# Performance work log

Measured on AMD Instinct MI355X. Metric: run time of the kernel, lower is better.

Reference implementation:

```python
import jax, jax.numpy as jnp
import numpy as np

N_NODES = 100000


def gcn_conv(x, W, b, src, dst, n_nodes):
    """PyG GCNConv: add self-loops, symmetric normalization, linear, scatter-add, bias."""
    xw = x @ W  # [N, out]
    loop = jnp.arange(n_nodes, dtype=src.dtype)
    src2 = jnp.concatenate([src, loop])  # sources (x_j gathered from here)
    dst2 = jnp.concatenate([dst, loop])  # targets (aggregation index)
    # degree (incl. self-loops) computed at target nodes, unit edge weights
    deg = jax.ops.segment_sum(jnp.ones_like(dst2, dtype=xw.dtype), dst2, num_segments=n_nodes)
    dinv = jnp.where(deg > 0, jax.lax.rsqrt(deg), 0.0)
    norm = dinv[src2] * dinv[dst2]  # [E+N]
    msg = xw[src2] * norm[:, None]  # [E+N, out]  (memory-bound gather)
    out = jax.ops.segment_sum(msg, dst2, num_segments=n_nodes)  # scatter-add
    return out + b


def setup_inputs() -> dict:
    key = jax.random.key(0)
    k1, k2, k3, k4 = jax.random.split(key, 4)
    F_IN, H, C = 128, 128, 64
    E = 1600000
    x = jax.random.normal(k1, (N_NODES, F_IN), dtype=jnp.float32)
    edge_index = jax.random.randint(k2, (2, E), 0, N_NODES, dtype=jnp.int64)
    # Glorot init like PyG GCNConv
    s1 = float(np.sqrt(6.0 / (F_IN + H)))
    s2 = float(np.sqrt(6.0 / (H + C)))
    W1 = jax.random.uniform(k3, (F_IN, H), jnp.float32, -s1, s1)
    W2 = jax.random.uniform(k4, (H, C), jnp.float32, -s2, s2)
    b1 = jnp.zeros((H,), jnp.float32)
    b2 = jnp.zeros((C,), jnp.float32)
    return {"x": x, "edge_index": edge_index, "W1": W1, "b1": b1, "W2": W2, "b2": b2}


def reference(x, edge_index, W1, b1, W2, b2):
    src, dst = edge_index[0], edge_index[1]
    h = gcn_conv(x, W1, b1, src, dst, N_NODES)
    h = jax.nn.relu(h)  # dropout p=0.0 -> identity
    h = gcn_conv(h, W2, b2, src, dst, N_NODES)
    return jax.nn.log_softmax(h, axis=1)
```

## Files before the change

### kernel.cpp

```cpp
#include <hip/hip_runtime.h>
#include <cmath>


#define THREADS 256
#define BSHIFT 8
#define MAXB 512
#define PADSLACK 1792

__device__ __forceinline__ unsigned short f2bf(float f) {
    union { float f; unsigned u; } v; v.f = f;
    unsigned r = v.u + 0x7FFFu + ((v.u >> 16) & 1u);
    return (unsigned short)(r >> 16);
}
__device__ __forceinline__ float bf_lo(unsigned u) {
    union { unsigned u; float f; } v; v.u = u << 16; return v.f;
}
__device__ __forceinline__ float bf_hi(unsigned u) {
    union { unsigned u; float f; } v; v.u = u & 0xFFFF0000u; return v.f;
}

__global__ __launch_bounds__(256) void k_bcount(const int* __restrict__ dst, int E, int B,
                                                int* __restrict__ bcnt) {
    __shared__ int lc[MAXB];
    for (int i = threadIdx.x; i < MAXB; i += 256) lc[i] = 0;
    __syncthreads();
    for (int e = blockIdx.x * blockDim.x + threadIdx.x; e < E; e += gridDim.x * blockDim.x)
        atomicAdd(&lc[dst[e] >> BSHIFT], 1);
    __syncthreads();
    for (int b = threadIdx.x; b < B; b += 256)
        if (lc[b]) atomicAdd(&bcnt[b], lc[b]);
}

__global__ void k_bscan(const int* __restrict__ bcnt, int B, int* __restrict__ boff) {
    __shared__ int sh[MAXB];
    const int t = threadIdx.x;
    int v = (t < B) ? bcnt[t] : 0;
    sh[t] = v; __syncthreads();
    for (int o = 1; o < MAXB; o <<= 1) {
        int add = (t >= o) ? sh[t - o] : 0;
        __syncthreads();
        sh[t] += add;
        __syncthreads();
    }
    if (t < B) boff[t] = sh[t] - v;
    if (t == B - 1) boff[B] = sh[t];
}

__global__ __launch_bounds__(256) void k_bscatter(const int* __restrict__ src,
                                                  const int* __restrict__ dst, int E, int B,
                                                  const int* __restrict__ boff,
                                                  int* __restrict__ bfill,
                                                  unsigned* __restrict__ pairs) {
    __shared__ int lc[MAXB];
    __shared__ int lbase[MAXB];
    const int tid = threadIdx.x;
    const int e0 = blockIdx.x * 8192;
    for (int i = tid; i < MAXB; i += 256) lc[i] = 0;
    __syncthreads();
#pragma unroll
    for (int k = 0; k < 32; k++) {
        int e = e0 + k * 256 + tid;
        if (e < E) atomicAdd(&lc[dst[e] >> BSHIFT], 1);
    }
    __syncthreads();
    for (int b = tid; b < B; b += 256)
        lbase[b] = lc[b] ? atomicAdd(&bfill[b], lc[b]) : 0;
    __syncthreads();
    for (int i = tid; i < MAXB; i += 256) lc[i] = 0;
    __syncthreads();
#pragma unroll
    for (int k = 0; k < 32; k++) {
        int e = e0 + k * 256 + tid;
        if (e < E) {
            int s = src[e], d = dst[e];
            int b = d >> BSHIFT;
            int r = atomicAdd(&lc[b], 1);
            pairs[(size_t)boff[b] + lbase[b] + r] =
                ((unsigned)(d & 255) << 24) | (unsigned)s;
        }
    }
}

__global__ __launch_bounds__(256) void k_bbuild(const unsigned* __restrict__ pairs,
                                                const int* __restrict__ boff, int N,
                                                int* __restrict__ deg,
                                                float* __restrict__ dinv,
                                                int* __restrict__ rowptr,
                                                int* __restrict__ csr_src) {
    __shared__ int ldeg[256], lex[256], lrank[256];
    const int b = blockIdx.x, tid = threadIdx.x;
    const int node0 = b << BSHIFT;
    const int base = boff[b];
    const int pbase = base + b * PADSLACK;
    const int cnt_e = boff[b + 1] - base;
    ldeg[tid] = 0;
    __syncthreads();
    for (int e = tid; e < cnt_e; e += 256)
        atomicAdd(&ldeg[pairs[base + e] >> 24], 1);
    __syncthreads();
    int v = ldeg[tid];
    int pd = (v + 7) & ~7;
    lex[tid] = pd; __syncthreads();
    for (int o = 1; o < 256; o <<= 1) {
        int add = (tid >= o) ? lex[tid - o] : 0;
        __syncthreads();
        lex[tid] += add;
        __syncthreads();
    }
    int pexcl = lex[tid] - pd;
    if (node0 + tid < N) {
        deg[node0 + tid] = v;
        dinv[node0 + tid] = rsqrtf((float)(v + 1));
        rowptr[node0 + tid] = pbase + pexcl;
    }
    __syncthreads();
    lex[tid] = pexcl;
    lrank[tid] = 0;
    __syncthreads();
    for (int e = tid; e < cnt_e; e += 256) {
        unsigned p = pairs[base + e];
        int loc = p >> 24;
        int r = atomicAdd(&lrank[loc], 1);
        csr_src[pbase + lex[loc] + r] = (int)(p & 0xFFFFFFu);
    }
    for (int p = v; p < pd; p++)
        csr_src[pbase + pexcl + p] = N;
}

__global__ void k_castW(const float* __restrict__ W1, const float* __restrict__ W2,
                        unsigned short* __restrict__ Wt1, unsigned short* __restrict__ Wt2) {
    int idx = blockIdx.x * blockDim.x + threadIdx.x;
    if (idx < 16384) {
        int n = idx >> 7, k = idx & 127;
        Wt1[idx] = f2bf(W1[k * 128 + n]);
    } else if (idx < 16384 + 8192) {
        int t = idx - 16384;
        int n = t >> 7, k = t & 127;
        Wt2[t] = f2bf(W2[k * 64 + n]);
    }
}

typedef __attribute__((ext_vector_type(8))) short bf16x8;
typedef __attribute__((ext_vector_type(4))) float f32x4;

template <int NC, bool A_BF16>
__global__ __launch_bounds__(256) void k_gemm_mfma(const void* __restrict__ Av,
                                                   const unsigned short* __restrict__ Wt,
                                                   const float* __restrict__ dinv,
                                                   unsigned short* __restrict__ Out,
                                                   unsigned short* __restrict__ zrow,
                                                   int M) {
    constexpr int KP = 136;
    __shared__ __align__(16) short As[64 * KP];
    __shared__ __align__(16) short Bs[NC * KP];
    const int tid = threadIdx.x;
    const int row0 = blockIdx.x * 64;

    if (blockIdx.x == 0 && tid < NC) zrow[tid] = 0;

    if (A_BF16) {
        const unsigned short* A = (const unsigned short*)Av;
#pragma unroll
        for (int q = 0; q < 4; q++) {
            int f = tid + 256 * q;
            int r = f >> 4, c = (f & 15) * 8;
            uint4 v = make_uint4(0, 0, 0, 0);
            if (row0 + r < M) v = *(const uint4*)&A[(size_t)(row0 + r) * 128 + c];
            *(uint4*)&As[r * KP + c] = v;
        }
    } else {
        const float* A = (const float*)Av;
#pragma unroll
        for (int q = 0; q < 8; q++) {
            int f = tid + 256 * q;
            int r = f >> 5, c = (f & 31) * 4;
            float4 v = make_float4(0.f, 0.f, 0.f, 0.f);
            if (row0 + r < M) v = *(const float4*)&A[(size_t)(row0 + r) * 128 + c];
            ushort4 o;
            o.x = f2bf(v.x); o.y = f2bf(v.y); o.z = f2bf(v.z); o.w = f2bf(v.w);
            *(ushort4*)&As[r * KP + c] = o;
        }
    }
    for (int f = tid; f < NC * 16; f += 256) {
        int n = f >> 4, c = (f & 15) * 8;
        *(uint4*)&Bs[n * KP + c] = *(const uint4*)&Wt[n * 128 + c];
    }
    __syncthreads();

    const int wave = tid >> 6, lane = tid & 63;
    const int m = lane & 15, quad = lane >> 4;
    constexpr int CT = NC / 16;
    f32x4 acc[CT] = {};
    const short* arow = &As[(16 * wave + m) * KP + quad * 8];
    const short* brow = &Bs[m * KP + quad * 8];
#pragma unroll
    for (int k0 = 0; k0 < 128; k0 += 32) {
        bf16x8 a = *(const bf16x8*)&arow[k0];
#pragma unroll
        for (int c = 0; c < CT; c++) {
            bf16x8 b = *(const bf16x8*)&brow[(size_t)c * 16 * KP + k0];
            acc[c] = __builtin_amdgcn_mfma_f32_16x16x32_bf16(a, b, acc[c], 0, 0, 0);
        }
    }

    __syncthreads();
    short* Cs = As;
    const int rbase = 16 * wave + quad * 4;
    float dv[4];
#pragma unroll
    for (int r = 0; r < 4; r++) {
        int gr = row0 + rbase + r;
        dv[r] = dinv[gr < M ? gr : 0];
    }
#pragma unroll
    for (int c = 0; c < CT; c++)
#pragma unroll
        for (int r = 0; r < 4; r++)
            Cs[(rbase + r) * NC + 16 * c + m] = (short)f2bf(acc[c][r] * dv[r]);
    __syncthreads();
    for (int f = tid; f < 64 * NC / 8; f += 256) {
        int r = f / (NC / 8), c = (f % (NC / 8)) * 8;
        if (row0 + r < M)
            *(uint4*)&Out[(size_t)(row0 + r) * NC + c] = *(const uint4*)&Cs[r * NC + c];
    }
}

__global__ __launch_bounds__(256) void k_agg128b(const int* __restrict__ csr_src,
                                                 const int* __restrict__ rowptr,
                                                 const int* __restrict__ cnt,
                                                 const float* __restrict__ dinv,
                                                 const unsigned* __restrict__ xw,
                                                 const float* __restrict__ bias,
                                                 unsigned* __restrict__ h1, int N) {
    const int lane = threadIdx.x & 63;
    const int wid = (blockIdx.x * blockDim.x + threadIdx.x) >> 6;
    const int h = lane >> 5, sl = lane & 31;
    const int i = wid * 2 + h;
    if (i >= N) return;
    const float di = dinv[i];
    uint2 u = *(const uint2*)&xw[(size_t)i * 64 + 2 * sl];
    float a0 = bf_lo(u.x), a1 = bf_hi(u.x);
    float a2 = bf_lo(u.y), a3 = bf_hi(u.y);
    const int start = rowptr[i];
    const int pc = (cnt[i] + 7) & ~7;
    int s[8];
#pragma unroll
    for (int k = 0; k < 8; k++) s[k] = csr_src[start + k];
    for (int j = 0; j < pc; j += 8) {
        uint2 uu[8];
#pragma unroll
        for (int k = 0; k < 8; k++) uu[k] = *(const uint2*)&xw[(size_t)s[k] * 64 + 2 * sl];
#pragma unroll
        for (int k = 0; k < 8; k++) s[k] = csr_src[start + j + 8 + k];
#pragma unroll
        for (int k = 0; k < 8; k++) {
            a0 += bf_lo(uu[k].x); a1 += bf_hi(uu[k].x);
            a2 += bf_lo(uu[k].y); a3 += bf_hi(uu[k].y);
        }
    }
    float4 b = *(const float4*)&bias[4 * sl];
    float r0 = fmaxf(di * a0 + b.x, 0.f);
    float r1 = fmaxf(di * a1 + b.y, 0.f);
    float r2 = fmaxf(di * a2 + b.z, 0.f);
    float r3 = fmaxf(di * a3 + b.w, 0.f);
    uint2 o;
    o.x = (unsigned)f2bf(r0) | ((unsigned)f2bf(r1) << 16);
    o.y = (unsigned)f2bf(r2) | ((unsigned)f2bf(r3) << 16);
    *(uint2*)&h1[(size_t)i * 64 + 2 * sl] = o;
}

__global__ __launch_bounds__(256) void k_agg64b(const int* __restrict__ csr_src,
                                                const int* __restrict__ rowptr,
                                                const int* __restrict__ cnt,
                                                const float* __restrict__ dinv,
                                                const unsigned* __restrict__ xw,
                                                const float* __restrict__ bias,
                                                float* __restrict__ out, int N) {
    const int lane = threadIdx.x & 63;
    const int wid = (blockIdx.x * blockDim.x + threadIdx.x) >> 6;
    const int h = lane >> 5;
    const int q = (lane >> 4) & 1;
    const int sl = lane & 15;
    const int i = wid * 2 + h;
    if (i >= N) return;
    const float di = dinv[i];
    float a0 = 0.f, a1 = 0.f, a2 = 0.f, a3 = 0.f;
    if (q == 0) {
        uint2 u = *(const uint2*)&xw[(size_t)i * 32 + 2 * sl];
        a0 = bf_lo(u.x); a1 = bf_hi(u.x); a2 = bf_lo(u.y); a3 = bf_hi(u.y);
    }
    const int start = rowptr[i];
    const int pc = (cnt[i] + 7) & ~7;
    int s[4];
#pragma unroll
    for (int k = 0; k < 4; k++) s[k] = csr_src[start + q + 2 * k];
    for (int e = 0; e < pc; e += 8) {
        uint2 uu[4];
#pragma unroll
        for (int k = 0; k < 4; k++) uu[k] = *(const uint2*)&xw[(size_t)s[k] * 32 + 2 * sl];
#pragma unroll
        for (int k = 0; k < 4; k++) s[k] = csr_src[start + e + 8 + q + 2 * k];
#pragma unroll
        for (int k = 0; k < 4; k++) {
            a0 += bf_lo(uu[k].x); a1 += bf_hi(uu[k].x);
            a2 += bf_lo(uu[k].y); a3 += bf_hi(uu[k].y);
        }
    }
    a0 += __shfl_xor(a0, 16); a1 += __shfl_xor(a1, 16);
    a2 += __shfl_xor(a2, 16); a3 += __shfl_xor(a3, 16);
    float4 b = *(const float4*)&bias[4 * sl];
    float v0 = di * a0 + b.x, v1 = di * a1 + b.y;
    float v2 = di * a2 + b.z, v3 = di * a3 + b.w;
    float m = fmaxf(fmaxf(v0, v1), fmaxf(v2, v3));
#pragma unroll
    for (int o = 8; o > 0; o >>= 1) m = fmaxf(m, __shfl_xor(m, o));
    float s2 = expf(v0 - m) + expf(v1 - m) + expf(v2 - m) + expf(v3 - m);
#pragma unroll
    for (int o = 8; o > 0; o >>= 1) s2 += __shfl_xor(s2, o);
    float ls = m + logf(s2);
    if (q == 0)
        *(float4*)&out[(size_t)i * 64 + 4 * sl] =
            make_float4(v0 - ls, v1 - ls, v2 - ls, v3 - ls);
}

extern "C" void kernel_launch(void* const* d_in, const int* in_sizes, int n_in,
                              void* d_out, int out_size, void* d_ws, size_t ws_size,
                              hipStream_t stream) {
    const float* x  = (const float*)d_in[0];
    const int*   ei = (const int*)d_in[1];
    const float* W1 = (const float*)d_in[2];
    const float* b1 = (const float*)d_in[3];
    const float* W2 = (const float*)d_in[4];
    const float* b2 = (const float*)d_in[5];

    const int N = in_sizes[0] / 128;
    const int E = in_sizes[1] / 2;
    const int* src = ei;
    const int* dst = ei + E;
    const int B = (N + 255) >> BSHIFT;

    char* ws = (char*)d_ws;
    size_t off = 0;
    auto alloc = [&](size_t bytes) {
        void* p = ws + off;
        off += (bytes + 255) & ~(size_t)255;
        return p;
    };
    int*            bcnt    = (int*)alloc(MAXB * 4 * 2);
    int*            bfill   = bcnt + MAXB;
    int*            boff    = (int*)alloc((MAXB + 1) * 4);
    int*            deg     = (int*)alloc((size_t)N * 4);
    float*          dinv    = (float*)alloc((size_t)N * 4);
    int*            rowptr  = (int*)alloc((size_t)N * 4);
    int*            csr_src = (int*)alloc(((size_t)E + (size_t)B * PADSLACK + 64) * 4);
    unsigned*       pairs   = (unsigned*)alloc((size_t)E * 4);
    unsigned short* Wt1     = (unsigned short*)alloc(128 * 128 * 2);
    unsigned short* Wt2     = (unsigned short*)alloc(64 * 128 * 2);
    unsigned short* xw1     = (unsigned short*)alloc((size_t)(N + 1) * 128 * 2);
    unsigned short* h1      = (unsigned short*)alloc((size_t)N * 128 * 2);
    unsigned short* hw2     = xw1;
    float*          out     = (float*)d_out;

    hipMemsetAsync(bcnt, 0, MAXB * 4 * 2, stream);

    k_bcount<<<512, THREADS, 0, stream>>>(dst, E, B, bcnt);
    k_bscan<<<1, MAXB, 0, stream>>>(bcnt, B, boff);
    k_bscatter<<<(E + 8191) / 8192, THREADS, 0, stream>>>(src, dst, E, B, boff, bfill, pairs);
    k_bbuild<<<B, THREADS, 0, stream>>>(pairs, boff, N, deg, dinv, rowptr, csr_src);

    k_castW<<<96, THREADS, 0, stream>>>(W1, W2, Wt1, Wt2);

    const int aggBlocks = (N + 7) / 8;

    k_gemm_mfma<128, false><<<(N + 63) / 64, THREADS, 0, stream>>>(
        x, Wt1, dinv, xw1, xw1 + (size_t)N * 128, N);
    k_agg128b<<<aggBlocks, THREADS, 0, stream>>>(
        csr_src, rowptr, deg, dinv, (const unsigned*)xw1, b1, (unsigned*)h1, N);

    k_gemm_mfma<64, true><<<(N + 63) / 64, THREADS, 0, stream>>>(
        h1, Wt2, dinv, hw2, hw2 + (size_t)N * 64, N);
    k_agg64b<<<aggBlocks, THREADS, 0, stream>>>(
        csr_src, rowptr, deg, dinv, (const unsigned*)hw2, b2, out, N);
}
```

Baseline: 287.3 us.

## Store CSR byte offsets, widen aggregation loads, feed GEMM A directly from registers

The CSR build now stores each source index pre-shifted as a byte offset into the bf16 feature table, so the gather kernels skip the index multiply. Both aggregation kernels switch to 16-byte loads with 16 or 8 lanes per node, so each wave handles 4 or 8 nodes; in the second layer this also removes the split-edge cross-lane shuffle. The MFMA GEMM loads its A fragments straight from global memory into registers instead of staging them through LDS, and reuses the B buffer for the output tile. The aim is fewer, wider memory transactions and less LDS traffic, at the cost of more registers and less coalesced A loads.

New measurement: 275.0 us. -4.3%, faster.

```diff
diff --git a/kernel.cpp b/kernel.cpp
--- a/kernel.cpp
+++ b/kernel.cpp
@@ -86,7 +86,7 @@
                                                 int* __restrict__ deg,
                                                 float* __restrict__ dinv,
                                                 int* __restrict__ rowptr,
-                                                int* __restrict__ csr_src) {
+                                                unsigned* __restrict__ csr_off) {
     __shared__ int ldeg[256], lex[256], lrank[256];
     const int b = blockIdx.x, tid = threadIdx.x;
     const int node0 = b << BSHIFT;
@@ -121,10 +121,10 @@
         unsigned p = pairs[base + e];
         int loc = p >> 24;
         int r = atomicAdd(&lrank[loc], 1);
-        csr_src[pbase + lex[loc] + r] = (int)(p & 0xFFFFFFu);
+        csr_off[pbase + lex[loc] + r] = (p & 0xFFFFFFu) << 8;
     }
     for (int p = v; p < pd; p++)
-        csr_src[pbase + pexcl + p] = N;
+        csr_off[pbase + pexcl + p] = ((unsigned)N) << 8;
 }
 
 __global__ void k_castW(const float* __restrict__ W1, const float* __restrict__ W2,
@@ -151,60 +151,58 @@
                                                    unsigned short* __restrict__ zrow,
                                                    int M) {
     constexpr int KP = 136;
-    __shared__ __align__(16) short As[64 * KP];
     __shared__ __align__(16) short Bs[NC * KP];
     const int tid = threadIdx.x;
     const int row0 = blockIdx.x * 64;
 
     if (blockIdx.x == 0 && tid < NC) zrow[tid] = 0;
 
-    if (A_BF16) {
-        const unsigned short* A = (const unsigned short*)Av;
-#pragma unroll
-        for (int q = 0; q < 4; q++) {
-            int f = tid + 256 * q;
-            int r = f >> 4, c = (f & 15) * 8;
-            uint4 v = make_uint4(0, 0, 0, 0);
-            if (row0 + r < M) v = *(const uint4*)&A[(size_t)(row0 + r) * 128 + c];
-            *(uint4*)&As[r * KP + c] = v;
-        }
-    } else {
-        const float* A = (const float*)Av;
-#pragma unroll
-        for (int q = 0; q < 8; q++) {
-            int f = tid + 256 * q;
-            int r = f >> 5, c = (f & 31) * 4;
-            float4 v = make_float4(0.f, 0.f, 0.f, 0.f);
-            if (row0 + r < M) v = *(const float4*)&A[(size_t)(row0 + r) * 128 + c];
-            ushort4 o;
-            o.x = f2bf(v.x); o.y = f2bf(v.y); o.z = f2bf(v.z); o.w = f2bf(v.w);
-            *(ushort4*)&As[r * KP + c] = o;
-        }
-    }
     for (int f = tid; f < NC * 16; f += 256) {
         int n = f >> 4, c = (f & 15) * 8;
         *(uint4*)&Bs[n * KP + c] = *(const uint4*)&Wt[n * 128 + c];
     }
-    __syncthreads();
 
     const int wave = tid >> 6, lane = tid & 63;
     const int m = lane & 15, quad = lane >> 4;
+    const int row = row0 + 16 * wave + m;
+    const int rowc = row < M ? row : (M - 1);
+
+    bf16x8 afr[4];
+    if (A_BF16) {
+        const unsigned short* A = (const unsigned short*)Av;
+#pragma unroll
+        for (int k = 0; k < 4; k++)
+            afr[k] = *(const bf16x8*)&A[(size_t)rowc * 128 + quad * 8 + 32 * k];
+    } else {
+        const float* A = (const float*)Av;
+#pragma unroll
+        for (int k = 0; k < 4; k++) {
+            float4 lo = *(const float4*)&A[(size_t)rowc * 128 + quad * 8 + 32 * k];
+            float4 hi = *(const float4*)&A[(size_t)rowc * 128 + quad * 8 + 32 * k + 4];
+            bf16x8 a;
+            a[0] = (short)f2bf(lo.x); a[1] = (short)f2bf(lo.y);
+            a[2] = (short)f2bf(lo.z); a[3] = (short)f2bf(lo.w);
+            a[4] = (short)f2bf(hi.x); a[5] = (short)f2bf(hi.y);
+            a[6] = (short)f2bf(hi.z); a[7] = (short)f2bf(hi.w);
+            afr[k] = a;
+        }
+    }
+    __syncthreads();
+
     constexpr int CT = NC / 16;
     f32x4 acc[CT] = {};
-    const short* arow = &As[(16 * wave + m) * KP + quad * 8];
     const short* brow = &Bs[m * KP + quad * 8];
 #pragma unroll
-    for (int k0 = 0; k0 < 128; k0 += 32) {
-        bf16x8 a = *(const bf16x8*)&arow[k0];
+    for (int k = 0; k < 4; k++) {
 #pragma unroll
         for (int c = 0; c < CT; c++) {
-            bf16x8 b = *(const bf16x8*)&brow[(size_t)c * 16 * KP + k0];
-            acc[c] = __builtin_amdgcn_mfma_f32_16x16x32_bf16(a, b, acc[c], 0, 0, 0);
-        }
-    }
-
-    __syncthreads();
-    short* Cs = As;
+            bf16x8 b = *(const bf16x8*)&brow[(size_t)c * 16 * KP + 32 * k];
+            acc[c] = __builtin_amdgcn_mfma_f32_16x16x32_bf16(afr[k], b, acc[c], 0, 0, 0);
+        }
+    }
+
+    __syncthreads();
+    short* Cs = Bs;
     const int rbase = 16 * wave + quad * 4;
     float dv[4];
 #pragma unroll
@@ -225,102 +223,113 @@
     }
 }
 
-__global__ __launch_bounds__(256) void k_agg128b(const int* __restrict__ csr_src,
+__global__ __launch_bounds__(256) void k_agg128b(const unsigned* __restrict__ csr_off,
                                                  const int* __restrict__ rowptr,
                                                  const int* __restrict__ cnt,
                                                  const float* __restrict__ dinv,
-                                                 const unsigned* __restrict__ xw,
+                                                 const unsigned char* __restrict__ xwb,
                                                  const float* __restrict__ bias,
                                                  unsigned* __restrict__ h1, int N) {
     const int lane = threadIdx.x & 63;
     const int wid = (blockIdx.x * blockDim.x + threadIdx.x) >> 6;
-    const int h = lane >> 5, sl = lane & 31;
-    const int i = wid * 2 + h;
+    const int g = lane >> 4, sl = lane & 15;
+    const int i = wid * 4 + g;
     if (i >= N) return;
     const float di = dinv[i];
-    uint2 u = *(const uint2*)&xw[(size_t)i * 64 + 2 * sl];
-    float a0 = bf_lo(u.x), a1 = bf_hi(u.x);
-    float a2 = bf_lo(u.y), a3 = bf_hi(u.y);
+    const int slb = sl * 16;
+    uint4 u = *(const uint4*)(xwb + ((size_t)i << 8) + slb);
+    float a0 = bf_lo(u.x), a1 = bf_hi(u.x), a2 = bf_lo(u.y), a3 = bf_hi(u.y);
+    float a4 = bf_lo(u.z), a5 = bf_hi(u.z), a6 = bf_lo(u.w), a7 = bf_hi(u.w);
     const int start = rowptr[i];
     const int pc = (cnt[i] + 7) & ~7;
-    int s[8];
-#pragma unroll
-    for (int k = 0; k < 8; k++) s[k] = csr_src[start + k];
+    unsigned s[8];
+#pragma unroll
+    for (int k = 0; k < 8; k++) s[k] = csr_off[start + k];
     for (int j = 0; j < pc; j += 8) {
-        uint2 uu[8];
-#pragma unroll
-        for (int k = 0; k < 8; k++) uu[k] = *(const uint2*)&xw[(size_t)s[k] * 64 + 2 * sl];
-#pragma unroll
-        for (int k = 0; k < 8; k++) s[k] = csr_src[start + j + 8 + k];
+        uint4 uu[8];
+#pragma unroll
+        for (int k = 0; k < 8; k++) uu[k] = *(const uint4*)(xwb + s[k] + slb);
+#pragma unroll
+        for (int k = 0; k < 8; k++) s[k] = csr_off[start + j + 8 + k];
 #pragma unroll
         for (int k = 0; k < 8; k++) {
             a0 += bf_lo(uu[k].x); a1 += bf_hi(uu[k].x);
             a2 += bf_lo(uu[k].y); a3 += bf_hi(uu[k].y);
-        }
-    }
-    float4 b = *(const float4*)&bias[4 * sl];
-    float r0 = fmaxf(di * a0 + b.x, 0.f);
-    float r1 = fmaxf(di * a1 + b.y, 0.f);
-    float r2 = fmaxf(di * a2 + b.z, 0.f);
-    float r3 = fmaxf(di * a3 + b.w, 0.f);
-    uint2 o;
+            a4 += bf_lo(uu[k].z); a5 += bf_hi(uu[k].z);
+            a6 += bf_lo(uu[k].w); a7 += bf_hi(uu[k].w);
+        }
+    }
+    float4 b0 = *(const float4*)&bias[8 * sl];
+    float4 b1 = *(const float4*)&bias[8 * sl + 4];
+    float r0 = fmaxf(di * a0 + b0.x, 0.f);
+    float r1 = fmaxf(di * a1 + b0.y, 0.f);
+    float r2 = fmaxf(di * a2 + b0.z, 0.f);
+    float r3 = fmaxf(di * a3 + b0.w, 0.f);
+    float r4 = fmaxf(di * a4 + b1.x, 0.f);
+    float r5 = fmaxf(di * a5 + b1.y, 0.f);
+    float r6 = fmaxf(di * a6 + b1.z, 0.f);
+    float r7 = fmaxf(di * a7 + b1.w, 0.f);
+    uint4 o;
     o.x = (unsigned)f2bf(r0) | ((unsigned)f2bf(r1) << 16);
     o.y = (unsigned)f2bf(r2) | ((unsigned)f2bf(r3) << 16);
-    *(uint2*)&h1[(size_t)i * 64 + 2 * sl] = o;
-}
-
-__global__ __launch_bounds__(256) void k_agg64b(const int* __restrict__ csr_src,
+    o.z = (unsigned)f2bf(r4) | ((unsigned)f2bf(r5) << 16);
+    o.w = (unsigned)f2bf(r6) | ((unsigned)f2bf(r7) << 16);
+    *(uint4*)&h1[(size_t)i * 64 + 4 * sl] = o;
+}
+
+__global__ __launch_bounds__(256) void k_agg64b(const unsigned* __restrict__ csr_off,
                                                 const int* __restrict__ rowptr,
                                                 const int* __restrict__ cnt,
                                                 const float* __restrict__ dinv,
-                                                const unsigned* __restrict__ xw,
+                                                const unsigned char* __restrict__ xwb,
                                                 const float* __restrict__ bias,
                                                 float* __restrict__ out, int N) {
     const int lane = threadIdx.x & 63;
     const int wid = (blockIdx.x * blockDim.x + threadIdx.x) >> 6;
-    const int h = lane >> 5;
-    const int q = (lane >> 4) & 1;
-    const int sl = lane & 15;
-    const int i = wid * 2 + h;
+    const int g = lane >> 3, sl = lane & 7;
+    const int i = wid * 8 + g;
     if (i >= N) return;
     const float di = dinv[i];
-    float a0 = 0.f, a1 = 0.f, a2 = 0.f, a3 = 0.f;
-    if (q == 0) {
-        uint2 u = *(const uint2*)&xw[(size_t)i * 32 + 2 * sl];
-        a0 = bf_lo(u.x); a1 = bf_hi(u.x); a2 = bf_lo(u.y); a3 = bf_hi(u.y);
-    }
+    const int slb = sl * 16;
+    uint4 u = *(const uint4*)(xwb + ((size_t)i << 7) + slb);
+    float a0 = bf_lo(u.x), a1 = bf_hi(u.x), a2 = bf_lo(u.y), a3 = bf_hi(u.y);
+    float a4 = bf_lo(u.z), a5 = bf_hi(u.z), a6 = bf_lo(u.w), a7 = bf_hi(u.w);
     const int start = rowptr[i];
     const int pc = (cnt[i] + 7) & ~7;
-    int s[4];
-#pragma unroll
-    for (int k = 0; k < 4; k++) s[k] = csr_src[start + q + 2 * k];
-    for (int e = 0; e < pc; e += 8) {
-        uint2 uu[4];
-#pragma unroll
-        for (int k = 0; k < 4; k++) uu[k] = *(const uint2*)&xw[(size_t)s[k] * 32 + 2 * sl];
-#pragma unroll
-        for (int k = 0; k < 4; k++) s[k] = csr_src[start + e + 8 + q + 2 * k];
-#pragma unroll
-        for (int k = 0; k < 4; k++) {
+    unsigned s[8];
+#pragma unroll
+    for (int k = 0; k < 8; k++) s[k] = csr_off[start + k];
+    for (int j = 0; j < pc; j += 8) {
+        uint4 uu[8];
+#pragma unroll
+        for (int k = 0; k < 8; k++) uu[k] = *(const uint4*)(xwb + (s[k] >> 1) + slb);
+#pragma unroll
+        for (int k = 0; k < 8; k++) s[k] = csr_off[start + j + 8 + k];
+#pragma unroll
+        for (int k = 0; k < 8; k++) {
             a0 += bf_lo(uu[k].x); a1 += bf_hi(uu[k].x);
             a2 += bf_lo(uu[k].y); a3 += bf_hi(uu[k].y);
-        }
-    }
-    a0 += __shfl_xor(a0, 16); a1 += __shfl_xor(a1, 16);
-    a2 += __shfl_xor(a2, 16); a3 += __shfl_xor(a3, 16);
-    float4 b = *(const float4*)&bias[4 * sl];
-    float v0 = di * a0 + b.x, v1 = di * a1 + b.y;
-    float v2 = di * a2 + b.z, v3 = di * a3 + b.w;
-    float m = fmaxf(fmaxf(v0, v1), fmaxf(v2, v3));
-#pragma unroll
-    for (int o = 8; o > 0; o >>= 1) m = fmaxf(m, __shfl_xor(m, o));
-    float s2 = expf(v0 - m) + expf(v1 - m) + expf(v2 - m) + expf(v3 - m);
-#pragma unroll
-    for (int o = 8; o > 0; o >>= 1) s2 += __shfl_xor(s2, o);
+            a4 += bf_lo(uu[k].z); a5 += bf_hi(uu[k].z);
+            a6 += bf_lo(uu[k].w); a7 += bf_hi(uu[k].w);
+        }
+    }
+    float4 b0 = *(const float4*)&bias[8 * sl];
+    float4 b1 = *(const float4*)&bias[8 * sl + 4];
+    float v0 = di * a0 + b0.x, v1 = di * a1 + b0.y;
+    float v2 = di * a2 + b0.z, v3 = di * a3 + b0.w;
+    float v4 = di * a4 + b1.x, v5 = di * a5 + b1.y;
+    float v6 = di * a6 + b1.z, v7 = di * a7 + b1.w;
+    float m = fmaxf(fmaxf(fmaxf(v0, v1), fmaxf(v2, v3)),
+                    fmaxf(fmaxf(v4, v5), fmaxf(v6, v7)));
+#pragma unroll
+    for (int o = 4; o > 0; o >>= 1) m = fmaxf(m, __shfl_xor(m, o));
+    float s2 = expf(v0 - m) + expf(v1 - m) + expf(v2 - m) + expf(v3 - m) +
+               expf(v4 - m) + expf(v5 - m) + expf(v6 - m) + expf(v7 - m);
+#pragma unroll
+    for (int o = 4; o > 0; o >>= 1) s2 += __shfl_xor(s2, o);
     float ls = m + logf(s2);
-    if (q == 0)
-        *(float4*)&out[(size_t)i * 64 + 4 * sl] =
-            make_float4(v0 - ls, v1 - ls, v2 - ls, v3 - ls);
+    *(float4*)&out[(size_t)i * 64 + 8 * sl] = make_float4(v0 - ls, v1 - ls, v2 - ls, v3 - ls);
+    *(float4*)&out[(size_t)i * 64 + 8 * sl + 4] = make_float4(v4 - ls, v5 - ls, v6 - ls, v7 - ls);
 }
 
 extern "C" void kernel_launch(void* const* d_in, const int* in_sizes, int n_in,
@@ -352,7 +361,7 @@
     int*            deg     = (int*)alloc((size_t)N * 4);
     float*          dinv    = (float*)alloc((size_t)N * 4);
     int*            rowptr  = (int*)alloc((size_t)N * 4);
-    int*            csr_src = (int*)alloc(((size_t)E + (size_t)B * PADSLACK + 64) * 4);
+    unsigned*       csr_off = (unsigned*)alloc(((size_t)E + (size_t)B * PADSLACK + 64) * 4);
     unsigned*       pairs   = (unsigned*)alloc((size_t)E * 4);
     unsigned short* Wt1     = (unsigned short*)alloc(128 * 128 * 2);
     unsigned short* Wt2     = (unsigned short*)alloc(64 * 128 * 2);
@@ -366,19 +375,20 @@
     k_bcount<<<512, THREADS, 0, stream>>>(dst, E, B, bcnt);
     k_bscan<<<1, MAXB, 0, stream>>>(bcnt, B, boff);
     k_bscatter<<<(E + 8191) / 8192, THREADS, 0, stream>>>(src, dst, E, B, boff, bfill, pairs);
-    k_bbuild<<<B, THREADS, 0, stream>>>(pairs, boff, N, deg, dinv, rowptr, csr_src);
+    k_bbuild<<<B, THREADS, 0, stream>>>(pairs, boff, N, deg, dinv, rowptr, csr_off);
 
     k_castW<<<96, THREADS, 0, stream>>>(W1, W2, Wt1, Wt2);
 
-    const int aggBlocks = (N + 7) / 8;
+    const int agg128Blocks = (N + 15) / 16;
+    const int agg64Blocks  = (N + 31) / 32;
 
     k_gemm_mfma<128, false><<<(N + 63) / 64, THREADS, 0, stream>>>(
         x, Wt1, dinv, xw1, xw1 + (size_t)N * 128, N);
-    k_agg128b<<<aggBlocks, THREADS, 0, stream>>>(
-        csr_src, rowptr, deg, dinv, (const unsigned*)xw1, b1, (unsigned*)h1, N);
+    k_agg128b<<<agg128Blocks, THREADS, 0, stream>>>(
+        csr_off, rowptr, deg, dinv, (const unsigned char*)xw1, b1, (unsigned*)h1, N);
 
     k_gemm_mfma<64, true><<<(N + 63) / 64, THREADS, 0, stream>>>(
         h1, Wt2, dinv, hw2, hw2 + (size_t)N * 64, N);
-    k_agg64b<<<aggBlocks, THREADS, 0, stream>>>(
-        csr_src, rowptr, deg, dinv, (const unsigned*)hw2, b2, out, N);
-}
+    k_agg64b<<<agg64Blocks, THREADS, 0, stream>>>(
+        csr_off, rowptr, deg, dinv, (const unsigned char*)hw2, b2, out, N);
+}
```
